# Kernel optimization log

Measured on AMD Instinct MI355X. Metric: run time of the kernel, lower is better.

## Reference

```python
import jax, jax.numpy as jnp
import numpy as np

B, S, D = 8, 2048, 1024

def setup_inputs() -> dict:
    key = jax.random.key(0)
    k1, k2 = jax.random.split(key)
    x = jax.random.normal(k1, (B, S, D), dtype=jnp.float32)
    # nn.Linear(dim, dim, bias=False) weight: [out, in]
    W = jax.random.normal(k2, (D, D), dtype=jnp.float32) * (1.0 / np.sqrt(D))
    return {"x": x, "W": W}

def reference(x, W):
    d = x.shape[-1]
    scale = 1.0 / jnp.sqrt(jnp.float32(d))
    # scores: [B, S, S]
    scores = jnp.einsum('bqd,bkd->bqk', x, x) * scale
    S_len = x.shape[-2]
    causal = jnp.tril(jnp.ones((S_len, S_len), dtype=bool))  # keep lower triangle incl. diag
    scores = jnp.where(causal[None, :, :], scores, -jnp.inf)
    attn_w = jax.nn.softmax(scores, axis=-1)
    attn = jnp.einsum('bqk,bkd->bqd', attn_w, x)
    # nn.Linear: y = attn @ W.T
    return jnp.einsum('bqd,ed->bqe', attn, W)
```

## Files before the change

kernel.cpp:

```cpp
#include <hip/hip_runtime.h>

typedef __attribute__((ext_vector_type(8))) __bf16 bf16x8;
typedef __attribute__((ext_vector_type(4))) float floatx4;

static __device__ __forceinline__ floatx4 mfma16(bf16x8 a, bf16x8 b, floatx4 c) {
  return __builtin_amdgcn_mfma_f32_16x16x32_bf16(a, b, c, 0, 0, 0);
}

static __device__ __forceinline__ unsigned short f2b_bits(float f) {
  __bf16 h = (__bf16)f;
  return __builtin_bit_cast(unsigned short, h);
}

static __device__ __forceinline__ void stage16(const void* g, void* l) {
  __builtin_amdgcn_global_load_lds(
      (__attribute__((address_space(1))) void*)(unsigned long long)g,
      (__attribute__((address_space(3))) void*)(unsigned int)(unsigned long long)l,
      16, 0, 0);
}

#define VM6B() asm volatile("s_waitcnt vmcnt(6)\n\ts_barrier" ::: "memory")
#define VM3B() asm volatile("s_waitcnt vmcnt(3)\n\ts_barrier" ::: "memory")
#define VM0B() asm volatile("s_waitcnt vmcnt(0)\n\ts_barrier" ::: "memory")
#define BAR()  asm volatile("s_barrier" ::: "memory")


__global__ __launch_bounds__(256) void cast_kernel(const float4* __restrict__ x,
                                                   const float4* __restrict__ w,
                                                   uint4* __restrict__ xb,
                                                   uint4* __restrict__ wb,
                                                   float4* __restrict__ lsum) {
  __shared__ unsigned char sl[32768];
  const int st = blockIdx.x, tid = threadIdx.x;
  if (st < 1088) {
    const float4* src = (st < 1024) ? x + (size_t)st * 4096 : w + (size_t)(st - 1024) * 4096;
    uint4* dst = (st < 1024) ? xb + (size_t)st * 2048 : wb + (size_t)(st - 1024) * 2048;
#pragma unroll
    for (int it = 0; it < 16; ++it) {
      const int row = it, c4 = tid;
      float4 v = src[row * 256 + c4];
      ushort4 o;
      o.x = f2b_bits(v.x); o.y = f2b_bits(v.y); o.z = f2b_bits(v.z); o.w = f2b_bits(v.w);
      *(ushort4*)(sl + row * 2048 + ((c4 * 8) ^ ((row & 7) << 4))) = o;
    }
    __syncthreads();
#pragma unroll
    for (int it = 0; it < 8; ++it) {
      const int o = it * 4096 + tid * 16;
      const int c = o >> 10, l = (o >> 4) & 63;
      const int row = l & 15, kg = l >> 4;
      uint4 v = *(const uint4*)(sl + row * 2048 + ((c * 64 + kg * 16) ^ ((row & 7) << 4)));
      dst[o >> 4] = v;
    }
  } else {
    const float4 z = {0.0f, 0.0f, 0.0f, 0.0f};
#pragma unroll
    for (int it = 0; it < 4; ++it) lsum[(st - 1088) * 1024 + it * 256 + tid] = z;
  }
}


__global__ __launch_bounds__(512, 2) void zq_fused(const unsigned short* __restrict__ xb,
                                                   const unsigned short* __restrict__ wb,
                                                   unsigned short* __restrict__ zT,
                                                   unsigned short* __restrict__ P,
                                                   float* __restrict__ lsum) {
  extern __shared__ bf16x8 lds[];
  bf16x8* ldsA = lds;
  bf16x8* ldsB = lds + 1536;
  const int tid = threadIdx.x, wid = tid >> 6, lane = tid & 63;
  const int wr = wid >> 2, wc = wid & 3, lr = lane & 15, lq = lane >> 4;
  const int g = blockIdx.x;
  const bool is_qk = (g >= 512);

  const unsigned short* gA;
  const unsigned short* gB0;
  const unsigned short* gB1;
  int b, mt, ntl, rt, ct;
  if (!is_qk) {
    b = g & 7;
    const int gg = g >> 3;
    mt = gg >> 2; ntl = gg & 3;
    gA = xb + ((size_t)b * 4096 + (mt * 8 + wid) * 32) * 512 + lane * 8;
    gB0 = wb + (size_t)((ntl * 16 + wid) * 32) * 512 + lane * 8;
    gB1 = wb + (size_t)((ntl * 16 + wid + 8) * 32) * 512 + lane * 8;
  } else {
    const int h = g - 512;
    b = h & 7;
    const int idx = h >> 3;
    int m = (int)((sqrtf(4.0f * idx + 1.0f) - 1.0f) * 0.5f);
    while ((m + 1) * (m + 2) <= idx) ++m;
    while (m * (m + 1) > idx) --m;
    const int rem = idx - m * (m + 1);
    rt = 2 * m + (rem > m);
    ct = rem - (rem > m ? (m + 1) : 0);
    gA = xb + ((size_t)b * 4096 + (rt * 8 + wid) * 32) * 512 + lane * 8;
    gB0 = xb + ((size_t)b * 4096 + (ct * 16 + wid) * 32) * 512 + lane * 8;
    gB1 = xb + ((size_t)b * 4096 + (ct * 16 + wid + 8) * 32) * 512 + lane * 8;
  }

  floatx4 acc[4][4] = {};

#pragma unroll
  for (int t = 0; t < 2; ++t) {
    stage16(gA + t * 512, &ldsA[t * 512 + wid * 64]);
    stage16(gB0 + t * 512, &ldsB[t * 1024 + wid * 64]);
    stage16(gB1 + t * 512, &ldsB[t * 1024 + (wid + 8) * 64]);
  }

#pragma unroll
  for (int kt = 0; kt < 32; ++kt) {
    const int cb = kt % 3;
    if (kt + 2 < 32) {
      const int sb = (kt + 2) % 3;
      stage16(gA + (kt + 2) * 512, &ldsA[sb * 512 + wid * 64]);
      stage16(gB0 + (kt + 2) * 512, &ldsB[sb * 1024 + wid * 64]);
      stage16(gB1 + (kt + 2) * 512, &ldsB[sb * 1024 + (wid + 8) * 64]);
      VM6B();
    } else if (kt + 1 < 32) {
      VM3B();
    } else {
      VM0B();
    }
    bf16x8 a_[4], b_[4];
#pragma unroll
    for (int i = 0; i < 4; ++i) a_[i] = ldsA[cb * 512 + (wr * 4 + i) * 64 + lane];
#pragma unroll
    for (int j = 0; j < 4; ++j) b_[j] = ldsB[cb * 1024 + (wc * 4 + j) * 64 + lane];
#pragma unroll
    for (int i = 0; i < 4; ++i)
#pragma unroll
      for (int j = 0; j < 4; ++j) acc[i][j] = mfma16(a_[i], b_[j], acc[i][j]);
    BAR();
  }

  if (!is_qk) {
#pragma unroll
    for (int i = 0; i < 4; ++i) {
      const int s0 = mt * 128 + wr * 64 + i * 16 + lq * 4;
      const int s5 = s0 >> 5, s3 = (s0 >> 3) & 3, s7 = s0 & 7;
#pragma unroll
      for (int j = 0; j < 4; ++j) {
        const int e4 = ntl * 16 + wc * 4 + j;
        ushort4 o;
        o.x = f2b_bits(acc[i][j][0]); o.y = f2b_bits(acc[i][j][1]);
        o.z = f2b_bits(acc[i][j][2]); o.w = f2b_bits(acc[i][j][3]);
        *(ushort4*)(zT + ((size_t)b * 4096 + e4 * 64 + s5) * 512 + s3 * 128 + lr * 8 + s7) = o;
      }
    }
  } else {
    const int col128 = 2 * ct + (wc >> 1);
    if (col128 <= rt) {
      const bool diag = (col128 == rt);
      unsigned short* Pt =
          P + ((size_t)b * 136 + (size_t)(rt * (rt + 1) / 2 + col128)) * 16384;
      float* lsb = lsum + b * 2048 + rt * 128;
#pragma unroll
      for (int i = 0; i < 4; ++i) {
        const int row_l = wr * 64 + i * 16 + lq * 4;
        floatx4 rs = {0.0f, 0.0f, 0.0f, 0.0f};
#pragma unroll
        for (int j = 0; j < 4; ++j) {
          const int incol = (wc & 1) * 64 + j * 16 + lr;
          const int cbase = ((wr * 4 + i) * 4 + (wc & 1) * 2 + (j >> 1)) * 512 +
                            ((j * 2 + (lr >> 3)) & 3) * 128 + (lr & 7);
#pragma unroll
          for (int v = 0; v < 4; ++v) {
            float p = __expf(acc[i][j][v] * 0.03125f - 44.0f);
            if (diag && incol > row_l + v) p = 0.0f;
            Pt[cbase + (lq * 4 + v) * 8] = f2b_bits(p);
            rs[v] += p;
          }
        }
#pragma unroll
        for (int v = 0; v < 4; ++v) {
          float s = rs[v];
          s += __shfl_xor(s, 1);
          s += __shfl_xor(s, 2);
          s += __shfl_xor(s, 4);
          s += __shfl_xor(s, 8);
          if (lr == 0) atomicAdd(&lsb[row_l + v], s);
        }
      }
    }
  }
}

__global__ __launch_bounds__(512, 2) void pv_out(const unsigned short* __restrict__ P,
                                                 const unsigned short* __restrict__ zT,
                                                 const float* __restrict__ lsum,
                                                 float* __restrict__ out) {
  extern __shared__ bf16x8 lds[];
  bf16x8* ldsA = lds;
  bf16x8* ldsB = lds + 1536;
  const int tid = threadIdx.x, wid = tid >> 6, lane = tid & 63;
  const int wr = wid >> 2, wc = wid & 3, lr = lane & 15, lq = lane >> 4;
  const int g = blockIdx.x, b = g & 7, gg = g >> 3;
  const int q = gg >> 2;
  const int rt = (gg < 32) ? 15 - q : q - 8;
  const int ntl = gg & 3;
  const int NKT = (rt + 1) * 4;

  const unsigned short* pA =
      P + ((size_t)b * 136 + (size_t)(rt * (rt + 1) / 2)) * 16384 + (size_t)wid * 2048 + lane * 8;
  const unsigned short* gB0 = zT + ((size_t)b * 4096 + (ntl * 16 + wid) * 64) * 512 + lane * 8;
  const unsigned short* gB1 =
      zT + ((size_t)b * 4096 + (ntl * 16 + wid + 8) * 64) * 512 + lane * 8;
  floatx4 acc[4][4] = {};

#pragma unroll
  for (int t = 0; t < 2; ++t) {
    stage16(pA + (t >> 2) * 16384 + (t & 3) * 512, &ldsA[t * 512 + wid * 64]);
    stage16(gB0 + t * 512, &ldsB[t * 1024 + wid * 64]);
    stage16(gB1 + t * 512, &ldsB[t * 1024 + (wid + 8) * 64]);
  }

  int cb = 0, sb = 2;
  for (int kt = 0; kt < NKT; ++kt) {
    if (kt + 2 < NKT) {
      const int k2 = kt + 2;
      stage16(pA + (k2 >> 2) * 16384 + (k2 & 3) * 512, &ldsA[sb * 512 + wid * 64]);
      stage16(gB0 + k2 * 512, &ldsB[sb * 1024 + wid * 64]);
      stage16(gB1 + k2 * 512, &ldsB[sb * 1024 + (wid + 8) * 64]);
      VM6B();
    } else if (kt + 1 < NKT) {
      VM3B();
    } else {
      VM0B();
    }
    bf16x8 a_[4], b_[4];
#pragma unroll
    for (int i = 0; i < 4; ++i) a_[i] = ldsA[cb * 512 + (wr * 4 + i) * 64 + lane];
#pragma unroll
    for (int j = 0; j < 4; ++j) b_[j] = ldsB[cb * 1024 + (wc * 4 + j) * 64 + lane];
#pragma unroll
    for (int i = 0; i < 4; ++i)
#pragma unroll
      for (int j = 0; j < 4; ++j) acc[i][j] = mfma16(a_[i], b_[j], acc[i][j]);
    BAR();
    cb = (cb == 2) ? 0 : cb + 1;
    sb = (sb == 2) ? 0 : sb + 1;
  }

  const float* lsb = lsum + b * 2048 + rt * 128;
  float* outb = out + (size_t)b * 2097152;
#pragma unroll
  for (int i = 0; i < 4; ++i) {
    const int row_l = wr * 64 + i * 16 + lq * 4;
    floatx4 linv;
#pragma unroll
    for (int v = 0; v < 4; ++v) linv[v] = 1.0f / lsb[row_l + v];
#pragma unroll
    for (int j = 0; j < 4; ++j) {
      const int col = ntl * 256 + wc * 64 + j * 16 + lr;
#pragma unroll
      for (int v = 0; v < 4; ++v)
        __builtin_nontemporal_store(acc[i][j][v] * linv[v],
                                    &outb[(size_t)(rt * 128 + row_l + v) * 1024 + col]);
    }
  }
}

extern "C" void kernel_launch(void* const* d_in, const int* in_sizes, int n_in,
                              void* d_out, int out_size, void* d_ws, size_t ws_size,
                              hipStream_t stream) {
  const float* x = (const float*)d_in[0];
  const float* W = (const float*)d_in[1];
  float* out = (float*)d_out;
  char* ws = (char*)d_ws;
  unsigned short* xb = (unsigned short*)ws;
  unsigned short* zT = (unsigned short*)(ws + 33554432ull);
  unsigned short* P  = (unsigned short*)(ws + 67108864ull);
  unsigned short* wb = (unsigned short*)(ws + 67108864ull + 35651584ull + 65536ull);
  float* lsum = (float*)(ws + 67108864ull + 35651584ull);

  static bool attr_done = false;
  if (!attr_done) {
    (void)hipFuncSetAttribute(reinterpret_cast<const void*>(zq_fused),
                              hipFuncAttributeMaxDynamicSharedMemorySize, 73728);
    (void)hipFuncSetAttribute(reinterpret_cast<const void*>(pv_out),
                              hipFuncAttributeMaxDynamicSharedMemorySize, 73728);
    attr_done = true;
  }

  cast_kernel<<<1092, 256, 0, stream>>>((const float4*)x, (const float4*)W,
                                        (uint4*)xb, (uint4*)wb, (float4*)lsum);
  zq_fused<<<1088, 512, 73728, stream>>>(xb, wb, zT, P, lsum);
  pv_out<<<512, 512, 73728, stream>>>(P, zT, lsum, out);
}
```

Baseline: 233.2 us.

## Enlarge fused projection/QK tiles to 256x256 with doubled A staging

The fused z-projection and QK^T kernel now computes 256x256 output tiles per block instead of 128x256. Each wave holds 8x4 MFMA accumulators, A is staged as two 128-row halves, and LDS grows to 96KB, so the grid halves to 544 blocks and the causal triangle is indexed over 256-row tiles. This raises arithmetic intensity and cuts redundant global/LDS loads. In exchange it increases register pressure (128 accumulator floats per lane) and LDS use, which may lower occupancy, and fewer blocks means worse load balance across CUs.

```diff
diff --git a/kernel.cpp b/kernel.cpp
--- a/kernel.cpp
+++ b/kernel.cpp
@@ -19,7 +19,9 @@
       16, 0, 0);
 }
 
+#define VM8B() asm volatile("s_waitcnt vmcnt(8)\n\ts_barrier" ::: "memory")
 #define VM6B() asm volatile("s_waitcnt vmcnt(6)\n\ts_barrier" ::: "memory")
+#define VM4B() asm volatile("s_waitcnt vmcnt(4)\n\ts_barrier" ::: "memory")
 #define VM3B() asm volatile("s_waitcnt vmcnt(3)\n\ts_barrier" ::: "memory")
 #define VM0B() asm volatile("s_waitcnt vmcnt(0)\n\ts_barrier" ::: "memory")
 #define BAR()  asm volatile("s_barrier" ::: "memory")
@@ -59,7 +61,6 @@
   }
 }
 
-
 __global__ __launch_bounds__(512, 2) void zq_fused(const unsigned short* __restrict__ xb,
                                                    const unsigned short* __restrict__ wb,
                                                    unsigned short* __restrict__ zT,
@@ -67,43 +68,46 @@
                                                    float* __restrict__ lsum) {
   extern __shared__ bf16x8 lds[];
   bf16x8* ldsA = lds;
-  bf16x8* ldsB = lds + 1536;
+  bf16x8* ldsB = lds + 3072;
   const int tid = threadIdx.x, wid = tid >> 6, lane = tid & 63;
   const int wr = wid >> 2, wc = wid & 3, lr = lane & 15, lq = lane >> 4;
   const int g = blockIdx.x;
-  const bool is_qk = (g >= 512);
-
-  const unsigned short* gA;
+  const bool is_qk = (g >= 256);
+
+  const unsigned short* gA0;
+  const unsigned short* gA1;
   const unsigned short* gB0;
   const unsigned short* gB1;
-  int b, mt, ntl, rt, ct;
+  int b, mt, ntl, MT, NT;
   if (!is_qk) {
     b = g & 7;
     const int gg = g >> 3;
     mt = gg >> 2; ntl = gg & 3;
-    gA = xb + ((size_t)b * 4096 + (mt * 8 + wid) * 32) * 512 + lane * 8;
+    gA0 = xb + ((size_t)b * 4096 + (mt * 16 + wid) * 32) * 512 + lane * 8;
+    gA1 = gA0 + 131072;
     gB0 = wb + (size_t)((ntl * 16 + wid) * 32) * 512 + lane * 8;
-    gB1 = wb + (size_t)((ntl * 16 + wid + 8) * 32) * 512 + lane * 8;
+    gB1 = gB0 + 131072;
   } else {
-    const int h = g - 512;
+    const int h = g - 256;
     b = h & 7;
     const int idx = h >> 3;
-    int m = (int)((sqrtf(4.0f * idx + 1.0f) - 1.0f) * 0.5f);
-    while ((m + 1) * (m + 2) <= idx) ++m;
-    while (m * (m + 1) > idx) --m;
-    const int rem = idx - m * (m + 1);
-    rt = 2 * m + (rem > m);
-    ct = rem - (rem > m ? (m + 1) : 0);
-    gA = xb + ((size_t)b * 4096 + (rt * 8 + wid) * 32) * 512 + lane * 8;
-    gB0 = xb + ((size_t)b * 4096 + (ct * 16 + wid) * 32) * 512 + lane * 8;
-    gB1 = xb + ((size_t)b * 4096 + (ct * 16 + wid + 8) * 32) * 512 + lane * 8;
-  }
-
-  floatx4 acc[4][4] = {};
+    int m = (int)((sqrtf(8.0f * idx + 1.0f) - 1.0f) * 0.5f);
+    while ((m + 1) * (m + 2) / 2 <= idx) ++m;
+    while (m * (m + 1) / 2 > idx) --m;
+    MT = m;
+    NT = idx - m * (m + 1) / 2;
+    gA0 = xb + ((size_t)b * 4096 + (MT * 16 + wid) * 32) * 512 + lane * 8;
+    gA1 = gA0 + 131072;
+    gB0 = xb + ((size_t)b * 4096 + (NT * 16 + wid) * 32) * 512 + lane * 8;
+    gB1 = gB0 + 131072;
+  }
+
+  floatx4 acc[8][4] = {};
 
 #pragma unroll
   for (int t = 0; t < 2; ++t) {
-    stage16(gA + t * 512, &ldsA[t * 512 + wid * 64]);
+    stage16(gA0 + t * 512, &ldsA[t * 1024 + wid * 64]);
+    stage16(gA1 + t * 512, &ldsA[t * 1024 + (wid + 8) * 64]);
     stage16(gB0 + t * 512, &ldsB[t * 1024 + wid * 64]);
     stage16(gB1 + t * 512, &ldsB[t * 1024 + (wid + 8) * 64]);
   }
@@ -113,22 +117,23 @@
     const int cb = kt % 3;
     if (kt + 2 < 32) {
       const int sb = (kt + 2) % 3;
-      stage16(gA + (kt + 2) * 512, &ldsA[sb * 512 + wid * 64]);
+      stage16(gA0 + (kt + 2) * 512, &ldsA[sb * 1024 + wid * 64]);
+      stage16(gA1 + (kt + 2) * 512, &ldsA[sb * 1024 + (wid + 8) * 64]);
       stage16(gB0 + (kt + 2) * 512, &ldsB[sb * 1024 + wid * 64]);
       stage16(gB1 + (kt + 2) * 512, &ldsB[sb * 1024 + (wid + 8) * 64]);
-      VM6B();
+      VM8B();
     } else if (kt + 1 < 32) {
-      VM3B();
+      VM4B();
     } else {
       VM0B();
     }
-    bf16x8 a_[4], b_[4];
-#pragma unroll
-    for (int i = 0; i < 4; ++i) a_[i] = ldsA[cb * 512 + (wr * 4 + i) * 64 + lane];
+    bf16x8 a_[8], b_[4];
+#pragma unroll
+    for (int i = 0; i < 8; ++i) a_[i] = ldsA[cb * 1024 + (wr * 8 + i) * 64 + lane];
 #pragma unroll
     for (int j = 0; j < 4; ++j) b_[j] = ldsB[cb * 1024 + (wc * 4 + j) * 64 + lane];
 #pragma unroll
-    for (int i = 0; i < 4; ++i)
+    for (int i = 0; i < 8; ++i)
 #pragma unroll
       for (int j = 0; j < 4; ++j) acc[i][j] = mfma16(a_[i], b_[j], acc[i][j]);
     BAR();
@@ -136,8 +141,8 @@
 
   if (!is_qk) {
 #pragma unroll
-    for (int i = 0; i < 4; ++i) {
-      const int s0 = mt * 128 + wr * 64 + i * 16 + lq * 4;
+    for (int i = 0; i < 8; ++i) {
+      const int s0 = mt * 256 + wr * 128 + i * 16 + lq * 4;
       const int s5 = s0 >> 5, s3 = (s0 >> 3) & 3, s7 = s0 & 7;
 #pragma unroll
       for (int j = 0; j < 4; ++j) {
@@ -149,25 +154,26 @@
       }
     }
   } else {
-    const int col128 = 2 * ct + (wc >> 1);
-    if (col128 <= rt) {
-      const bool diag = (col128 == rt);
+    const int r128 = 2 * MT + wr;
+    const int c128 = 2 * NT + (wc >> 1);
+    if (c128 <= r128) {
+      const bool diag = (c128 == r128);
       unsigned short* Pt =
-          P + ((size_t)b * 136 + (size_t)(rt * (rt + 1) / 2 + col128)) * 16384;
-      float* lsb = lsum + b * 2048 + rt * 128;
-#pragma unroll
-      for (int i = 0; i < 4; ++i) {
-        const int row_l = wr * 64 + i * 16 + lq * 4;
+          P + ((size_t)b * 136 + (size_t)(r128 * (r128 + 1) / 2 + c128)) * 16384;
+      float* lsb = lsum + b * 2048 + r128 * 128;
+#pragma unroll
+      for (int i = 0; i < 8; ++i) {
+        const int q0 = i * 16 + lq * 4;
         floatx4 rs = {0.0f, 0.0f, 0.0f, 0.0f};
 #pragma unroll
         for (int j = 0; j < 4; ++j) {
           const int incol = (wc & 1) * 64 + j * 16 + lr;
-          const int cbase = ((wr * 4 + i) * 4 + (wc & 1) * 2 + (j >> 1)) * 512 +
+          const int cbase = (i * 4 + (wc & 1) * 2 + (j >> 1)) * 512 +
                             ((j * 2 + (lr >> 3)) & 3) * 128 + (lr & 7);
 #pragma unroll
           for (int v = 0; v < 4; ++v) {
             float p = __expf(acc[i][j][v] * 0.03125f - 44.0f);
-            if (diag && incol > row_l + v) p = 0.0f;
+            if (diag && incol > q0 + v) p = 0.0f;
             Pt[cbase + (lq * 4 + v) * 8] = f2b_bits(p);
             rs[v] += p;
           }
@@ -179,7 +185,7 @@
           s += __shfl_xor(s, 2);
           s += __shfl_xor(s, 4);
           s += __shfl_xor(s, 8);
-          if (lr == 0) atomicAdd(&lsb[row_l + v], s);
+          if (lr == 0) atomicAdd(&lsb[q0 + v], s);
         }
       }
     }
@@ -277,7 +283,7 @@
   static bool attr_done = false;
   if (!attr_done) {
     (void)hipFuncSetAttribute(reinterpret_cast<const void*>(zq_fused),
-                              hipFuncAttributeMaxDynamicSharedMemorySize, 73728);
+                              hipFuncAttributeMaxDynamicSharedMemorySize, 98304);
     (void)hipFuncSetAttribute(reinterpret_cast<const void*>(pv_out),
                               hipFuncAttributeMaxDynamicSharedMemorySize, 73728);
     attr_done = true;
@@ -285,6 +291,6 @@
 
   cast_kernel<<<1092, 256, 0, stream>>>((const float4*)x, (const float4*)W,
                                         (uint4*)xb, (uint4*)wb, (float4*)lsum);
-  zq_fused<<<1088, 512, 73728, stream>>>(xb, wb, zT, P, lsum);
+  zq_fused<<<544, 512, 98304, stream>>>(xb, wb, zT, P, lsum);
   pv_out<<<512, 512, 73728, stream>>>(P, zT, lsum, out);
 }
```

Result: slower. 240.4 us (+3.1%).
